# Optimization experiments

Measured on AMD Instinct MI355X. Metric: run time of the kernel, lower is better.

The kernel has to match this reference:

```python
import jax, jax.numpy as jnp
import numpy as np

D = 768        # TEXT_DIM
N = 50         # seq len (h,w = 1,50 in source)
HEADS = 8
LABEL_SIZE = 50
B = 512
EPS_COS = 1e-8
EPS_LN = 1e-5


def _egce(x, w):
    # EGCE source not provided in repo snippet; implemented as ECA-style efficient
    # gated channel excitation: GAP over HW -> 1D conv (k=3) over channels -> sigmoid gate.
    gap = x.mean(axis=(2, 3))                      # [b, c]
    p = jnp.pad(gap, ((0, 0), (1, 1)))
    att = jax.nn.sigmoid(w[0] * p[:, :-2] + w[1] * p[:, 1:-1] + w[2] * p[:, 2:])
    return x * att[:, :, None, None]


def _lstm(x, Wih, Whh, bih, bhh):
    # PyTorch single-layer batch_first LSTM, gate order i,f,g,o, zero init state.
    b, n, d = x.shape
    xg = jnp.einsum('bnd,gd->bng', x, Wih) + bih + bhh   # [b, n, 4d]
    def step(carry, xt):
        h, c = carry
        g = xt + h @ Whh.T
        i, f, gg, o = jnp.split(g, 4, axis=-1)
        c = jax.nn.sigmoid(f) * c + jax.nn.sigmoid(i) * jnp.tanh(gg)
        h = jax.nn.sigmoid(o) * jnp.tanh(c)
        return (h, c), h
    h0 = jnp.zeros((b, d), x.dtype)
    _, ys = jax.lax.scan(step, (h0, h0), jnp.swapaxes(xg, 0, 1))
    return jnp.swapaxes(ys, 0, 1)


def _cross_attn(q_in, kv_in, qW, qb, kW, kb, vW, vb):
    b, n, d = q_in.shape
    dh = d // HEADS
    q = (q_in @ qW.T + qb).reshape(b, n, HEADS, dh).transpose(0, 2, 1, 3)
    k = (kv_in @ kW.T + kb).reshape(b, -1, HEADS, dh).transpose(0, 2, 1, 3)
    v = (kv_in @ vW.T + vb).reshape(b, -1, HEADS, dh).transpose(0, 2, 1, 3)
    attn = jax.nn.softmax(jnp.einsum('bhqd,bhkd->bhqk', q, k) * dh ** -0.5, axis=-1)
    # NOTE: faithful to source: einsum('bhqk,bhvd->bhqd') sums k and v INDEPENDENTLY
    out = jnp.einsum('bhqk,bhvd->bhqd', attn, v)
    return out.transpose(0, 2, 1, 3).reshape(b, n, d)


def _ln(x, g, b):
    m = x.mean(-1, keepdims=True)
    v = ((x - m) ** 2).mean(-1, keepdims=True)
    return (x - m) * jax.lax.rsqrt(v + EPS_LN) * g + b


def setup_inputs() -> dict:
    key = jax.random.key(0)
    ks = jax.random.split(key, 24)
    s = 0.02
    def w(k, shape):
        return jax.random.normal(k, shape, jnp.float32) * s
    vis_emb = w(ks[0], (LABEL_SIZE + 1, D)).at[LABEL_SIZE].set(0.0)
    ac_emb = w(ks[1], (LABEL_SIZE + 1, D)).at[LABEL_SIZE].set(0.0)
    inp = {
        'text_embedding': jax.random.normal(ks[2], (B, N, D), jnp.float32),
        'visual_ids': jax.random.randint(ks[3], (B, N), 0, LABEL_SIZE),
        'acoustic_ids': jax.random.randint(ks[4], (B, N), 0, LABEL_SIZE),
        'vis_emb': vis_emb,
        'ac_emb': ac_emb,
        'egce_w': w(ks[5], (3,)) + 0.3,
        'lstm_Wih': w(ks[6], (4 * D, D)),
        'lstm_Whh': w(ks[7], (4 * D, D)),
        'lstm_bih': jnp.zeros((4 * D,), jnp.float32),
        'lstm_bhh': jnp.zeros((4 * D,), jnp.float32),
        'ln_g': jnp.ones((D,), jnp.float32),
        'ln_b': jnp.zeros((D,), jnp.float32),
        'concat_W': w(ks[8], (D, 3 * D)),
        'concat_b': jnp.zeros((D,), jnp.float32),
        'hybrid_W': w(ks[9], (D, 3 * D)),
        'hybrid_b': jnp.zeros((D,), jnp.float32),
        # stacked cross-attention params, index 0 = cross_att_t, 1 = cross_att_a, 2 = cross_att_v
        'ca_qW': w(ks[10], (3, D, D)), 'ca_qb': w(ks[11], (3, D)),
        'ca_kW': w(ks[12], (3, D, D)), 'ca_kb': w(ks[13], (3, D)),
        'ca_vW': w(ks[14], (3, D, D)), 'ca_vb': w(ks[15], (3, D)),
    }
    return inp


def _forward(text_embedding, vis_emb, ac_emb, egce_w, lstm_Wih, lstm_Whh,
             lstm_bih, lstm_bhh, ln_g, ln_b, concat_W, concat_b, hybrid_W,
             hybrid_b, ca_qW, ca_qb, ca_kW, ca_kb, ca_vW, ca_vb,
             visual_ids, acoustic_ids):
    b, n, c = text_embedding.shape
    visual_ = jax.nn.relu(vis_emb[visual_ids])
    acoustic_ = ac_emb[acoustic_ids]
    # faithful reshape (NOT transpose) [b,n,c] -> [b,c,1,n] -> egce -> [b,n,c]
    text = _egce(text_embedding.reshape(b, c, 1, n), egce_w).reshape(b, n, c)
    visual_ = _egce(visual_.reshape(b, c, 1, n), egce_w).reshape(b, n, c)
    acoustic_ = _egce(acoustic_.reshape(b, c, 1, n), egce_w).reshape(b, n, c)

    # ---- AFI (vectorized over batch via masks instead of Python loop) ----
    def cos(x, y):
        xm, ym = x.mean(1), y.mean(1)
        nx = jnp.maximum(jnp.sqrt((xm * xm).sum(-1)), EPS_COS)
        ny = jnp.maximum(jnp.sqrt((ym * ym).sum(-1)), EPS_COS)
        return (xm * ym).sum(-1) / (nx * ny)
    rtv, rta, rva = cos(text, visual_), cos(text, acoustic_), cos(visual_, acoustic_)
    delta = (rtv + rta + rva) / 3.0
    joint = (rtv + rta + rva) / 3.0   # identical to delta in source
    cat = jnp.concatenate([text, visual_, acoustic_], axis=-1)  # [b,n,3d]
    f_concat = cat @ concat_W.T + concat_b
    f_hybrid = cat @ hybrid_W.T + hybrid_b
    tv = _cross_attn(text, visual_, ca_qW[0], ca_qb[0], ca_kW[0], ca_kb[0], ca_vW[0], ca_vb[0])
    ta = _cross_attn(text, acoustic_, ca_qW[1], ca_qb[1], ca_kW[1], ca_kb[1], ca_vW[1], ca_vb[1])
    va = _cross_attn(visual_, acoustic_, ca_qW[2], ca_qb[2], ca_kW[2], ca_kb[2], ca_vW[2], ca_vb[2])
    f_cross = (tv + ta + va) / 3.0
    m1 = ((rtv > delta) & (rta > delta) & (rva > delta))[:, None, None]
    m2 = (joint > delta)[:, None, None]
    fusion = jnp.where(m1, f_concat, jnp.where(m2, f_hybrid, f_cross))
    # dropout is identity in eval mode

    shift = _ln(fusion + text, ln_g, ln_b)
    out = _lstm(shift, lstm_Wih, lstm_Whh, lstm_bih, lstm_bhh) + text
    return out


def reference(text_embedding, visual_ids, acoustic_ids, vis_emb, ac_emb, egce_w,
              lstm_Wih, lstm_Whh, lstm_bih, lstm_bhh, ln_g, ln_b, concat_W,
              concat_b, hybrid_W, hybrid_b, ca_qW, ca_qb, ca_kW, ca_kb, ca_vW, ca_vb):
    return _forward(text_embedding, vis_emb, ac_emb, egce_w, lstm_Wih, lstm_Whh,
                    lstm_bih, lstm_bhh, ln_g, ln_b, concat_W, concat_b, hybrid_W,
                    hybrid_b, ca_qW, ca_qb, ca_kW, ca_kb, ca_vW, ca_vb,
                    visual_ids, acoustic_ids)
```

## Files before the change

### kernel.cpp

```cpp
#include <hip/hip_runtime.h>
#include <hip/hip_bf16.h>
#include <math.h>

#define B 512
#define N 50
#define D 768
#define G4 3072
#define BN (B*N)
#define FLAT (N*D)
#define TCH 10
#define NCHUNK (N/TCH)
#define KC 1536

typedef __hip_bfloat16 bf16;
typedef short short8 __attribute__((ext_vector_type(8)));
typedef float floatx4 __attribute__((ext_vector_type(4)));

__device__ __forceinline__ float sigf(float x){ return 1.0f/(1.0f+expf(-x)); }
__device__ __forceinline__ float u2f(unsigned short u){ return __uint_as_float(((unsigned int)u)<<16); }
__device__ __forceinline__ unsigned short f2u(float f){ bf16 h=__float2bfloat16(f); return *(unsigned short*)&h; }

__global__ __launch_bounds__(256) void egce_att(
    const float* __restrict__ text, const int* __restrict__ vid, const int* __restrict__ aid,
    const float* __restrict__ vemb, const float* __restrict__ aemb, const float* __restrict__ egw,
    float* __restrict__ att_t, float* __restrict__ att_v, float* __restrict__ att_a){
  int b = blockIdx.x; int tid = threadIdx.x;
  __shared__ float gt[D+2], gv[D+2], ga[D+2];
  float w0 = egw[0], w1 = egw[1], w2 = egw[2];
  if(tid==0){ gt[0]=gv[0]=ga[0]=0.f; gt[D+1]=gv[D+1]=ga[D+1]=0.f; }
  const float* tb = text + (size_t)b*FLAT;
  const int* vb_ = vid + b*N; const int* ab_ = aid + b*N;
  for(int ch = tid; ch < D; ch += 256){
    float st=0.f, sv=0.f, sa=0.f;
    int j0 = ch*50;
    for(int p=0;p<50;p++){
      int j = j0+p; int n = j/D; int d = j - n*D;
      st += tb[j];
      float vv = vemb[vb_[n]*D + d]; sv += vv>0.f?vv:0.f;
      sa += aemb[ab_[n]*D + d];
    }
    gt[ch+1]=st*(1.f/50.f); gv[ch+1]=sv*(1.f/50.f); ga[ch+1]=sa*(1.f/50.f);
  }
  __syncthreads();
  for(int ch = tid; ch < D; ch += 256){
    att_t[b*D+ch] = sigf(w0*gt[ch]+w1*gt[ch+1]+w2*gt[ch+2]);
    att_v[b*D+ch] = sigf(w0*gv[ch]+w1*gv[ch+1]+w2*gv[ch+2]);
    att_a[b*D+ch] = sigf(w0*ga[ch]+w1*ga[ch+1]+w2*ga[ch+2]);
  }
}

__global__ __launch_bounds__(256) void gate_sums2(
    const int* __restrict__ vid, const int* __restrict__ aid,
    const float* __restrict__ vemb, const float* __restrict__ aemb,
    const float* __restrict__ att_v, const float* __restrict__ att_a,
    unsigned short* __restrict__ catAB){
  int b = blockIdx.x; int tid = threadIdx.x;
  float va[3]={0,0,0}, aa[3]={0,0,0};
  const float* Av = att_v + b*D; const float* Aa = att_a + b*D;
  for(int n=0;n<N;n++){
    int id_v = vid[b*N+n]; int id_a = aid[b*N+n];
    for(int q=0;q<3;q++){
      int d = q*256 + tid;
      int ch = (n*D + d)/50;
      float vv = vemb[id_v*D+d]; vv = vv>0.f?vv:0.f;
      va[q] += vv * Av[ch];
      aa[q] += aemb[id_a*D+d] * Aa[ch];
    }
  }
  for(int q=0;q<3;q++){
    int d=q*256+tid;
    catAB[(size_t)b*KC + d]     = f2u(va[q]);
    catAB[(size_t)b*KC + D + d] = f2u(aa[q]);
  }
}

__global__ __launch_bounds__(256) void prep_weights(
    const float* __restrict__ Wih, const float* __restrict__ Whh,
    const float* __restrict__ bih, const float* __restrict__ bhh,
    unsigned short* __restrict__ WihP, unsigned short* __restrict__ WhhP,
    float* __restrict__ bsum){
  int np = blockIdx.x;
  int dg = np>>2, g = np&3;
  size_t src = (size_t)(g*D+dg)*D;
  for(int k=threadIdx.x;k<D;k+=256){
    WihP[(size_t)np*D+k] = f2u(Wih[src+k]);
    WhhP[(size_t)np*D+k] = f2u(Whh[src+k]);
  }
  if(threadIdx.x==0) bsum[np] = bih[g*D+dg] + bhh[g*D+dg];
}

__global__ __launch_bounds__(256) void prep_fcross(
    const float* __restrict__ vW, const float* __restrict__ vb,
    unsigned short* __restrict__ WcB, float* __restrict__ fb){
  int n = blockIdx.x;
  const float* W0 = vW; const float* W1 = vW + D*D; const float* W2 = vW + 2*D*D;
  for(int k=threadIdx.x;k<D;k+=256){
    WcB[(size_t)n*KC + k]     = f2u(W0[(size_t)n*D+k]);
    WcB[(size_t)n*KC + D + k] = f2u(W1[(size_t)n*D+k] + W2[(size_t)n*D+k]);
  }
  if(threadIdx.x==0) fb[n] = 50.f*(vb[n]+vb[D+n]+vb[2*D+n]);
}

__global__ __launch_bounds__(256) void fcross_mfma(
    const unsigned short* __restrict__ catAB, const unsigned short* __restrict__ WcB,
    const float* __restrict__ fb, float* __restrict__ fcross){
  __shared__ unsigned short Ash[32*40];
  __shared__ unsigned short Bsh[64*40];
  int tid=threadIdx.x;
  int bx=blockIdx.x, by=blockIdx.y;
  int lane=tid&63, w=tid>>6;
  int l15=lane&15, lq=lane>>4;
  int arow=tid>>3, aseg=(tid&7)*4;
  int brow=tid>>2, bseg=(tid&3)*8;
  floatx4 acc0={},acc1={};
  const unsigned short* aG = catAB + (size_t)(by*32 + arow)*KC + aseg;
  const unsigned short* bG = WcB   + (size_t)(bx*64 + brow)*KC + bseg;
  for(int k0=0;k0<KC;k0+=32){
    *(uint2*)&Ash[arow*40 + aseg] = *(const uint2*)(aG + k0);
    *(uint4*)&Bsh[brow*40 + bseg] = *(const uint4*)(bG + k0);
    __syncthreads();
    short8 a0=*(const short8*)&Ash[l15*40 + lq*8];
    short8 a1=*(const short8*)&Ash[(16+l15)*40 + lq*8];
    short8 bb=*(const short8*)&Bsh[(w*16 + l15)*40 + lq*8];
    acc0=__builtin_amdgcn_mfma_f32_16x16x32_bf16(a0,bb,acc0,0,0,0);
    acc1=__builtin_amdgcn_mfma_f32_16x16x32_bf16(a1,bb,acc1,0,0,0);
    __syncthreads();
  }
  int n = bx*64 + w*16 + l15;
  float bias = fb[n];
  #pragma unroll
  for(int r=0;r<4;r++){
    int m0 = by*32 + lq*4 + r;
    fcross[(size_t)m0*D + n]      = (acc0[r] + bias)*(1.f/3.f);
    fcross[(size_t)(m0+16)*D + n] = (acc1[r] + bias)*(1.f/3.f);
  }
}

__global__ __launch_bounds__(256) void fuse_ln(
    const float* __restrict__ text, const float* __restrict__ att_t,
    const float* __restrict__ fcross, const float* __restrict__ lng,
    const float* __restrict__ lnb, bf16* __restrict__ shift){
  int row = blockIdx.x;
  int b = row/N, n = row - b*N;
  int tid=threadIdx.x;
  float v[3];
  for(int q=0;q<3;q++){
    int d=q*256+tid;
    int ch=(n*D+d)/50;
    v[q] = text[(size_t)row*D+d]*att_t[(size_t)b*D+ch] + fcross[(size_t)b*D+d];
  }
  __shared__ float red[256];
  red[tid]=v[0]+v[1]+v[2]; __syncthreads();
  for(int st=128;st>0;st>>=1){ if(tid<st) red[tid]+=red[tid+st]; __syncthreads(); }
  float m = red[0]*(1.f/768.f);
  __syncthreads();
  float s2=0.f;
  for(int q=0;q<3;q++){ float dl=v[q]-m; s2+=dl*dl; }
  red[tid]=s2; __syncthreads();
  for(int st=128;st>0;st>>=1){ if(tid<st) red[tid]+=red[tid+st]; __syncthreads(); }
  float var = red[0]*(1.f/768.f);
  float rs = 1.f/sqrtf(var+1e-5f);
  for(int q=0;q<3;q++){
    int d=q*256+tid;
    shift[(size_t)row*D+d]=__float2bfloat16((v[q]-m)*rs*lng[d]+lnb[d]);
  }
}

__global__ __launch_bounds__(256) void zero_init(float* __restrict__ cbuf, unsigned short* __restrict__ h0){
  size_t i=(size_t)blockIdx.x*256+threadIdx.x;
  if(i<(size_t)B*D){ cbuf[i]=0.f; h0[i]=0; }
}

__global__ __launch_bounds__(256) void xg_gemm_mfma(
    const unsigned short* __restrict__ shift, const unsigned short* __restrict__ WihP,
    const float* __restrict__ bsum, unsigned short* __restrict__ xgc, int c0){
  __shared__ unsigned short Ash[64*40];
  __shared__ unsigned short Bsh[64*40];
  int tid=threadIdx.x;
  int bx=blockIdx.x, by=blockIdx.y;
  int lane=tid&63, w=tid>>6;
  int wm=w&1, wn=w>>1;
  int srow=tid>>2, skg=(tid&3)*8;
  int l15=lane&15, lq=lane>>4;
  floatx4 acc[2][2]={};
  int R = by*64 + srow;
  int b = R/TCH; int tin = R - b*TCH;
  const unsigned short* aG = shift + ((size_t)b*N + c0 + tin)*D + skg;
  const unsigned short* bG = WihP + (size_t)(bx*64 + srow)*D + skg;
  for(int k0=0;k0<D;k0+=32){
    *(uint4*)&Ash[srow*40 + skg] = *(const uint4*)(aG + k0);
    *(uint4*)&Bsh[srow*40 + skg] = *(const uint4*)(bG + k0);
    __syncthreads();
    short8 a0=*(const short8*)&Ash[(wm*32 + l15)*40 + lq*8];
    short8 a1=*(const short8*)&Ash[(wm*32 + 16 + l15)*40 + lq*8];
    short8 b0=*(const short8*)&Bsh[(wn*32 + l15)*40 + lq*8];
    short8 b1=*(const short8*)&Bsh[(wn*32 + 16 + l15)*40 + lq*8];
    acc[0][0]=__builtin_amdgcn_mfma_f32_16x16x32_bf16(a0,b0,acc[0][0],0,0,0);
    acc[0][1]=__builtin_amdgcn_mfma_f32_16x16x32_bf16(a0,b1,acc[0][1],0,0,0);
    acc[1][0]=__builtin_amdgcn_mfma_f32_16x16x32_bf16(a1,b0,acc[1][0],0,0,0);
    acc[1][1]=__builtin_amdgcn_mfma_f32_16x16x32_bf16(a1,b1,acc[1][1],0,0,0);
    __syncthreads();
  }
  #pragma unroll
  for(int tm=0;tm<2;tm++){
    #pragma unroll
    for(int tn=0;tn<2;tn++){
      int n = bx*64 + wn*32 + tn*16 + l15;
      float bs = bsum[n];
      #pragma unroll
      for(int r=0;r<4;r++){
        int m = wm*32 + tm*16 + lq*4 + r;
        size_t Rg = (size_t)by*64 + m;
        xgc[Rg*G4 + n] = f2u(acc[tm][tn][r] + bs);
      }
    }
  }
}

__global__ __launch_bounds__(256) void lstm_step_mfma(
    const unsigned short* __restrict__ hprev, unsigned short* __restrict__ hnext,
    float* __restrict__ cbuf, const unsigned short* __restrict__ xgc,
    const unsigned short* __restrict__ WhhP,
    const float* __restrict__ text, const float* __restrict__ att_t,
    float* __restrict__ out, int t, int tin){
  __shared__ unsigned short Ash[32*40];
  __shared__ unsigned short Bsh[64*40];
  __shared__ float gbuf[32][65];
  int tid=threadIdx.x;
  int bx=blockIdx.x, by=blockIdx.y;
  int lane=tid&63, w=tid>>6;
  int l15=lane&15, lq=lane>>4;
  int arow=tid>>3, aseg=(tid&7)*4;
  int brow=tid>>2, bseg=(tid&3)*8;
  floatx4 acc0={},acc1={};
  const unsigned short* aG = hprev + (size_t)(by*32 + arow)*D + aseg;
  const unsigned short* bG = WhhP + (size_t)(bx*64 + brow)*D + bseg;
  for(int k0=0;k0<D;k0+=32){
    *(uint2*)&Ash[arow*40 + aseg] = *(const uint2*)(aG + k0);
    *(uint4*)&Bsh[brow*40 + bseg] = *(const uint4*)(bG + k0);
    __syncthreads();
    short8 a0=*(const short8*)&Ash[l15*40 + lq*8];
    short8 a1=*(const short8*)&Ash[(16+l15)*40 + lq*8];
    short8 bb=*(const short8*)&Bsh[(w*16 + l15)*40 + lq*8];
    acc0=__builtin_amdgcn_mfma_f32_16x16x32_bf16(a0,bb,acc0,0,0,0);
    acc1=__builtin_amdgcn_mfma_f32_16x16x32_bf16(a1,bb,acc1,0,0,0);
    __syncthreads();
  }
  {
    int n = w*16 + l15;
    #pragma unroll
    for(int r=0;r<4;r++){
      gbuf[lq*4+r][n]      = acc0[r];
      gbuf[16+lq*4+r][n]   = acc1[r];
    }
  }
  __syncthreads();
  for(int p=tid;p<512;p+=256){
    int bl=p>>4, dgl=p&15;
    int b=by*32+bl, dg=bx*16+dgl;
    size_t xr=((size_t)b*TCH + tin)*G4 + bx*64 + dgl*4;
    float gi=gbuf[bl][dgl*4+0] + u2f(xgc[xr+0]);
    float gf=gbuf[bl][dgl*4+1] + u2f(xgc[xr+1]);
    float gg=gbuf[bl][dgl*4+2] + u2f(xgc[xr+2]);
    float go=gbuf[bl][dgl*4+3] + u2f(xgc[xr+3]);
    float c_old=cbuf[(size_t)b*D+dg];
    float cn=sigf(gf)*c_old + sigf(gi)*tanhf(gg);
    float hn=sigf(go)*tanhf(cn);
    cbuf[(size_t)b*D+dg]=cn;
    hnext[(size_t)b*D+dg]=f2u(hn);
    size_t oidx=((size_t)b*N+t)*D+dg;
    int ch=(t*D+dg)/50;
    out[oidx]=hn + text[oidx]*att_t[(size_t)b*D+ch];
  }
}

extern "C" void kernel_launch(void* const* d_in, const int* in_sizes, int n_in,
                              void* d_out, int out_size, void* d_ws, size_t ws_size,
                              hipStream_t stream){
  const float* text=(const float*)d_in[0];
  const int*  vid =(const int*) d_in[1];
  const int*  aid =(const int*) d_in[2];
  const float* vemb=(const float*)d_in[3];
  const float* aemb=(const float*)d_in[4];
  const float* egw =(const float*)d_in[5];
  const float* Wih =(const float*)d_in[6];
  const float* Whh =(const float*)d_in[7];
  const float* bih =(const float*)d_in[8];
  const float* bhh =(const float*)d_in[9];
  const float* lng =(const float*)d_in[10];
  const float* lnb =(const float*)d_in[11];
  const float* vW  =(const float*)d_in[20];
  const float* vb  =(const float*)d_in[21];
  float* out = (float*)d_out;

  float* W = (float*)d_ws;
  const size_t S = (size_t)B*D;
  float* att_t = W;
  float* att_v = att_t + S;
  float* att_a = att_v + S;
  float* fcross= att_a + S;
  float* cbuf  = fcross + S;
  float* bsum  = cbuf + S;
  float* fb    = bsum + G4;
  unsigned short* WihP = (unsigned short*)(fb + D);
  unsigned short* WhhP = WihP + (size_t)G4*D;
  unsigned short* WcB  = WhhP + (size_t)G4*D;
  unsigned short* catAB= WcB + (size_t)D*KC;
  unsigned short* hA0  = catAB + (size_t)B*KC;
  unsigned short* hA1  = hA0 + S;
  bf16*  shift = (bf16*)(hA1 + S);
  unsigned short* xgc  = (unsigned short*)(shift + (size_t)BN*D);

  prep_weights<<<G4,256,0,stream>>>(Wih,Whh,bih,bhh,WihP,WhhP,bsum);
  prep_fcross<<<D,256,0,stream>>>(vW,vb,WcB,fb);
  egce_att<<<B,256,0,stream>>>(text,vid,aid,vemb,aemb,egw,att_t,att_v,att_a);
  gate_sums2<<<B,256,0,stream>>>(vid,aid,vemb,aemb,att_v,att_a,catAB);
  fcross_mfma<<<dim3(12,16),256,0,stream>>>(catAB,WcB,fb,fcross);
  fuse_ln<<<BN,256,0,stream>>>(text,att_t,fcross,lng,lnb,shift);
  zero_init<<<(unsigned)((S+255)/256),256,0,stream>>>(cbuf,hA0);

  int t=0;
  for(int c=0;c<NCHUNK;c++){
    xg_gemm_mfma<<<dim3(48, (B*TCH)/64),256,0,stream>>>((const unsigned short*)shift,WihP,bsum,xgc,c*TCH);
    for(int ti=0;ti<TCH;ti++,t++){
      unsigned short* hp = (t&1)? hA1 : hA0;
      unsigned short* hn = (t&1)? hA0 : hA1;
      lstm_step_mfma<<<dim3(48,16),256,0,stream>>>(hp,hn,cbuf,xgc,WhhP,text,att_t,out,t,ti);
    }
  }
}
```

Baseline: 1.464 ms.

## Fuse EGCE kernels with coalesced LDS staging and retile LSTM step without LDS

Merges the EGCE attention and gate-sum kernels into one block per batch row. The per-channel means are now computed from coalesced loads staged through shared memory instead of strided per-thread reads, and the attention vectors stay in LDS rather than round-tripping through global memory. Separately, the per-timestep LSTM kernel now reads MFMA fragments directly from global memory with no LDS staging or barriers. Each block covers 64 batch rows instead of 32, halving the grid and reusing each weight fragment across four MFMAs. The trade-off is more register pressure, fewer blocks per launch, and uncoalesced direct fragment loads that rely on cache hits.

Result: slower. 2.220 ms (+51.7%).

```diff
diff --git a/kernel.cpp b/kernel.cpp
--- a/kernel.cpp
+++ b/kernel.cpp
@@ -11,6 +11,7 @@
 #define TCH 10
 #define NCHUNK (N/TCH)
 #define KC 1536
+#define CCH 6400
 
 typedef __hip_bfloat16 bf16;
 typedef short short8 __attribute__((ext_vector_type(8)));
@@ -20,57 +21,59 @@
 __device__ __forceinline__ float u2f(unsigned short u){ return __uint_as_float(((unsigned int)u)<<16); }
 __device__ __forceinline__ unsigned short f2u(float f){ bf16 h=__float2bfloat16(f); return *(unsigned short*)&h; }
 
-__global__ __launch_bounds__(256) void egce_att(
+__global__ __launch_bounds__(256) void egce_fused(
     const float* __restrict__ text, const int* __restrict__ vid, const int* __restrict__ aid,
     const float* __restrict__ vemb, const float* __restrict__ aemb, const float* __restrict__ egw,
-    float* __restrict__ att_t, float* __restrict__ att_v, float* __restrict__ att_a){
-  int b = blockIdx.x; int tid = threadIdx.x;
+    float* __restrict__ att_t, unsigned short* __restrict__ catAB){
+  __shared__ float buf[CCH];
   __shared__ float gt[D+2], gv[D+2], ga[D+2];
-  float w0 = egw[0], w1 = egw[1], w2 = egw[2];
+  __shared__ float attvS[D], attaS[D];
+  __shared__ int vidS[N], aidS[N];
+  int b=blockIdx.x, tid=threadIdx.x;
+  if(tid<N){ vidS[tid]=vid[b*N+tid]; aidS[tid]=aid[b*N+tid]; }
   if(tid==0){ gt[0]=gv[0]=ga[0]=0.f; gt[D+1]=gv[D+1]=ga[D+1]=0.f; }
+  __syncthreads();
   const float* tb = text + (size_t)b*FLAT;
-  const int* vb_ = vid + b*N; const int* ab_ = aid + b*N;
-  for(int ch = tid; ch < D; ch += 256){
-    float st=0.f, sv=0.f, sa=0.f;
-    int j0 = ch*50;
-    for(int p=0;p<50;p++){
-      int j = j0+p; int n = j/D; int d = j - n*D;
-      st += tb[j];
-      float vv = vemb[vb_[n]*D + d]; sv += vv>0.f?vv:0.f;
-      sa += aemb[ab_[n]*D + d];
-    }
-    gt[ch+1]=st*(1.f/50.f); gv[ch+1]=sv*(1.f/50.f); ga[ch+1]=sa*(1.f/50.f);
+  for(int c=0;c<6;c++){
+    int j0=c*CCH;
+    for(int it=0;it<25;it++) buf[it*256+tid]=tb[j0+it*256+tid];
+    __syncthreads();
+    if(tid<128){ float s=0.f; for(int p=0;p<50;p++) s+=buf[tid*50+p]; gt[c*128+tid+1]=s*(1.f/50.f); }
+    __syncthreads();
+    for(int it=0;it<25;it++){ int j=j0+it*256+tid; int n=j/D, d=j-n*D;
+      float v=vemb[vidS[n]*D+d]; buf[it*256+tid]=v>0.f?v:0.f; }
+    __syncthreads();
+    if(tid<128){ float s=0.f; for(int p=0;p<50;p++) s+=buf[tid*50+p]; gv[c*128+tid+1]=s*(1.f/50.f); }
+    __syncthreads();
+    for(int it=0;it<25;it++){ int j=j0+it*256+tid; int n=j/D, d=j-n*D;
+      buf[it*256+tid]=aemb[aidS[n]*D+d]; }
+    __syncthreads();
+    if(tid<128){ float s=0.f; for(int p=0;p<50;p++) s+=buf[tid*50+p]; ga[c*128+tid+1]=s*(1.f/50.f); }
+    __syncthreads();
+  }
+  float w0=egw[0],w1=egw[1],w2=egw[2];
+  for(int ch=tid;ch<D;ch+=256){
+    att_t[(size_t)b*D+ch]=sigf(w0*gt[ch]+w1*gt[ch+1]+w2*gt[ch+2]);
+    attvS[ch]=sigf(w0*gv[ch]+w1*gv[ch+1]+w2*gv[ch+2]);
+    attaS[ch]=sigf(w0*ga[ch]+w1*ga[ch+1]+w2*ga[ch+2]);
   }
   __syncthreads();
-  for(int ch = tid; ch < D; ch += 256){
-    att_t[b*D+ch] = sigf(w0*gt[ch]+w1*gt[ch+1]+w2*gt[ch+2]);
-    att_v[b*D+ch] = sigf(w0*gv[ch]+w1*gv[ch+1]+w2*gv[ch+2]);
-    att_a[b*D+ch] = sigf(w0*ga[ch]+w1*ga[ch+1]+w2*ga[ch+2]);
-  }
-}
-
-__global__ __launch_bounds__(256) void gate_sums2(
-    const int* __restrict__ vid, const int* __restrict__ aid,
-    const float* __restrict__ vemb, const float* __restrict__ aemb,
-    const float* __restrict__ att_v, const float* __restrict__ att_a,
-    unsigned short* __restrict__ catAB){
-  int b = blockIdx.x; int tid = threadIdx.x;
   float va[3]={0,0,0}, aa[3]={0,0,0};
-  const float* Av = att_v + b*D; const float* Aa = att_a + b*D;
   for(int n=0;n<N;n++){
-    int id_v = vid[b*N+n]; int id_a = aid[b*N+n];
+    int idv=vidS[n], ida=aidS[n];
+    #pragma unroll
     for(int q=0;q<3;q++){
-      int d = q*256 + tid;
-      int ch = (n*D + d)/50;
-      float vv = vemb[id_v*D+d]; vv = vv>0.f?vv:0.f;
-      va[q] += vv * Av[ch];
-      aa[q] += aemb[id_a*D+d] * Aa[ch];
+      int d=q*256+tid;
+      int ch=(n*D+d)/50;
+      float vv=vemb[idv*D+d]; vv=vv>0.f?vv:0.f;
+      va[q]+=vv*attvS[ch];
+      aa[q]+=aemb[ida*D+d]*attaS[ch];
     }
   }
   for(int q=0;q<3;q++){
     int d=q*256+tid;
-    catAB[(size_t)b*KC + d]     = f2u(va[q]);
-    catAB[(size_t)b*KC + D + d] = f2u(aa[q]);
+    catAB[(size_t)b*KC+d]    =f2u(va[q]);
+    catAB[(size_t)b*KC+D+d]  =f2u(aa[q]);
   }
 }
 
@@ -217,47 +220,38 @@
   }
 }
 
-__global__ __launch_bounds__(256) void lstm_step_mfma(
+__global__ __launch_bounds__(256) void lstm_step2(
     const unsigned short* __restrict__ hprev, unsigned short* __restrict__ hnext,
     float* __restrict__ cbuf, const unsigned short* __restrict__ xgc,
     const unsigned short* __restrict__ WhhP,
     const float* __restrict__ text, const float* __restrict__ att_t,
     float* __restrict__ out, int t, int tin){
-  __shared__ unsigned short Ash[32*40];
-  __shared__ unsigned short Bsh[64*40];
-  __shared__ float gbuf[32][65];
+  __shared__ float gbuf[64][68];
   int tid=threadIdx.x;
   int bx=blockIdx.x, by=blockIdx.y;
   int lane=tid&63, w=tid>>6;
   int l15=lane&15, lq=lane>>4;
-  int arow=tid>>3, aseg=(tid&7)*4;
-  int brow=tid>>2, bseg=(tid&3)*8;
-  floatx4 acc0={},acc1={};
-  const unsigned short* aG = hprev + (size_t)(by*32 + arow)*D + aseg;
-  const unsigned short* bG = WhhP + (size_t)(bx*64 + brow)*D + bseg;
+  floatx4 acc[4]={};
+  const unsigned short* Bp = WhhP + (size_t)(bx*64 + w*16 + l15)*D + lq*8;
+  const unsigned short* Ap = hprev + (size_t)(by*64 + l15)*D + lq*8;
+  #pragma unroll 4
   for(int k0=0;k0<D;k0+=32){
-    *(uint2*)&Ash[arow*40 + aseg] = *(const uint2*)(aG + k0);
-    *(uint4*)&Bsh[brow*40 + bseg] = *(const uint4*)(bG + k0);
-    __syncthreads();
-    short8 a0=*(const short8*)&Ash[l15*40 + lq*8];
-    short8 a1=*(const short8*)&Ash[(16+l15)*40 + lq*8];
-    short8 bb=*(const short8*)&Bsh[(w*16 + l15)*40 + lq*8];
-    acc0=__builtin_amdgcn_mfma_f32_16x16x32_bf16(a0,bb,acc0,0,0,0);
-    acc1=__builtin_amdgcn_mfma_f32_16x16x32_bf16(a1,bb,acc1,0,0,0);
-    __syncthreads();
-  }
-  {
-    int n = w*16 + l15;
+    short8 bfr = *(const short8*)(Bp + k0);
     #pragma unroll
-    for(int r=0;r<4;r++){
-      gbuf[lq*4+r][n]      = acc0[r];
-      gbuf[16+lq*4+r][n]   = acc1[r];
+    for(int mi=0;mi<4;mi++){
+      short8 afr = *(const short8*)(Ap + (size_t)mi*16*D + k0);
+      acc[mi]=__builtin_amdgcn_mfma_f32_16x16x32_bf16(afr,bfr,acc[mi],0,0,0);
     }
   }
+  #pragma unroll
+  for(int mi=0;mi<4;mi++)
+    #pragma unroll
+    for(int r=0;r<4;r++)
+      gbuf[mi*16 + lq*4 + r][w*16 + l15] = acc[mi][r];
   __syncthreads();
-  for(int p=tid;p<512;p+=256){
+  for(int p=tid;p<1024;p+=256){
     int bl=p>>4, dgl=p&15;
-    int b=by*32+bl, dg=bx*16+dgl;
+    int b=by*64+bl, dg=bx*16+dgl;
     size_t xr=((size_t)b*TCH + tin)*G4 + bx*64 + dgl*4;
     float gi=gbuf[bl][dgl*4+0] + u2f(xgc[xr+0]);
     float gf=gbuf[bl][dgl*4+1] + u2f(xgc[xr+1]);
@@ -296,9 +290,7 @@
   float* W = (float*)d_ws;
   const size_t S = (size_t)B*D;
   float* att_t = W;
-  float* att_v = att_t + S;
-  float* att_a = att_v + S;
-  float* fcross= att_a + S;
+  float* fcross= att_t + S;
   float* cbuf  = fcross + S;
   float* bsum  = cbuf + S;
   float* fb    = bsum + G4;
@@ -313,8 +305,7 @@
 
   prep_weights<<<G4,256,0,stream>>>(Wih,Whh,bih,bhh,WihP,WhhP,bsum);
   prep_fcross<<<D,256,0,stream>>>(vW,vb,WcB,fb);
-  egce_att<<<B,256,0,stream>>>(text,vid,aid,vemb,aemb,egw,att_t,att_v,att_a);
-  gate_sums2<<<B,256,0,stream>>>(vid,aid,vemb,aemb,att_v,att_a,catAB);
+  egce_fused<<<B,256,0,stream>>>(text,vid,aid,vemb,aemb,egw,att_t,catAB);
   fcross_mfma<<<dim3(12,16),256,0,stream>>>(catAB,WcB,fb,fcross);
   fuse_ln<<<BN,256,0,stream>>>(text,att_t,fcross,lng,lnb,shift);
   zero_init<<<(unsigned)((S+255)/256),256,0,stream>>>(cbuf,hA0);
@@ -325,7 +316,7 @@
     for(int ti=0;ti<TCH;ti++,t++){
       unsigned short* hp = (t&1)? hA1 : hA0;
       unsigned short* hn = (t&1)? hA0 : hA1;
-      lstm_step_mfma<<<dim3(48,16),256,0,stream>>>(hp,hn,cbuf,xgc,WhhP,text,att_t,out,t,ti);
+      lstm_step2<<<dim3(48,8),256,0,stream>>>(hp,hn,cbuf,xgc,WhhP,text,att_t,out,t,ti);
     }
   }
 }
```
